# Performance work log

Measured on AMD Instinct MI355X. Metric: run time of the kernel, lower is better.

The kernel has to match this reference:

```python
import jax, jax.numpy as jnp
import numpy as np

PRESERVE_RATIO = 0.8
TEMPERATURE = 1.5


def setup_inputs() -> dict:
    key = jax.random.key(0)
    ks = jax.random.split(key, 8)
    B, C, H, W = 2, 64, 96, 96
    inter = C // 2
    bott = C // 4
    s = 0.02
    return {
        "x": jax.random.normal(ks[0], (B, C, H, W), dtype=jnp.float32),
        "g_w": jax.random.normal(ks[1], (inter, C), dtype=jnp.float32) * s,
        "theta_w": jax.random.normal(ks[2], (inter, C), dtype=jnp.float32) * s,
        "phi_w": jax.random.normal(ks[3], (inter, C), dtype=jnp.float32) * s,
        "W_w": jax.random.normal(ks[4], (C, inter), dtype=jnp.float32) * s,
        "cg1_w": jax.random.normal(ks[5], (bott, C), dtype=jnp.float32) * s,
        "cg1_b": jnp.zeros((bott,), dtype=jnp.float32),
        "cg2_w": jax.random.normal(ks[6], (C, bott), dtype=jnp.float32) * s,
        "cg2_b": jnp.zeros((C,), dtype=jnp.float32),
    }


def reference(x, g_w, theta_w, phi_w, W_w, cg1_w, cg1_b, cg2_w, cg2_b):
    B, C, H, W = x.shape
    N = H * W
    # color gate: global avg pool -> 1x1 conv -> relu -> 1x1 conv -> sigmoid
    pooled = jnp.mean(x, axis=(2, 3))                       # [B, C]
    h = jax.nn.relu(pooled @ cg1_w.T + cg1_b)               # [B, C//4]
    gate = jax.nn.sigmoid(h @ cg2_w.T + cg2_b)              # [B, C]

    xf = x.reshape(B, C, N)                                 # [B, C, N]
    g_x = jnp.einsum('ic,bcn->bni', g_w, xf)                # [B, N, I]
    theta = jnp.einsum('ic,bcn->bni', theta_w, xf)          # [B, N, I]
    phi = jnp.einsum('ic,bcn->bin', phi_w, xf)              # [B, I, N]

    affinity = jnp.einsum('bni,bim->bnm', theta, phi) / TEMPERATURE  # [B, N, N]
    affinity = jax.nn.softmax(affinity, axis=-1)
    y = jnp.einsum('bnm,bmi->bni', affinity, g_x)           # [B, N, I]
    y = jnp.einsum('ci,bni->bcn', W_w, y).reshape(B, C, H, W)
    y = y * gate[:, :, None, None] * PRESERVE_RATIO
    return x + y
```

## Files before the change

### kernel.cpp

```cpp
#include <hip/hip_runtime.h>

#define N_TOK 9216
#define C_DIM 64
#define I_DIM 32
#define BOT 16
#define B_SZ 2
#define N_TILES 144

typedef short bf16x8 __attribute__((ext_vector_type(8)));
typedef float f32x4 __attribute__((ext_vector_type(4)));
typedef float f32x16 __attribute__((ext_vector_type(16)));

#define KST 36
#define VST 68

__device__ __forceinline__ unsigned packbf(float a, float b) {
  return __builtin_amdgcn_perm(__float_as_uint(b), __float_as_uint(a), 0x07060302u);
}
__device__ __forceinline__ unsigned short bftrunc(float f) {
  return (unsigned short)(__float_as_uint(f) >> 16);
}
__device__ __forceinline__ float bflo(unsigned u) {
  return __uint_as_float(u << 16);
}
__device__ __forceinline__ float bfhi(unsigned u) {
  return __uint_as_float(u & 0xffff0000u);
}

__global__ __launch_bounds__(256) void proj_pool_kernel(
    const float* __restrict__ x, const float* __restrict__ g_w,
    const float* __restrict__ theta_w, const float* __restrict__ phi_w,
    unsigned short* __restrict__ Q, unsigned short* __restrict__ K,
    unsigned short* __restrict__ VT, float* __restrict__ pooled) {
  if (blockIdx.x >= 216) {
    int bc = blockIdx.x - 216;
    const float* p = x + (size_t)bc * N_TOK;
    float s = 0.f;
    for (int t = threadIdx.x; t < N_TOK; t += 256) s += p[t];
#pragma unroll
    for (int off = 32; off >= 1; off >>= 1) s += __shfl_down(s, off, 64);
    __shared__ float red[4];
    int wid = threadIdx.x >> 6, lane = threadIdx.x & 63;
    if (lane == 0) red[wid] = s;
    __syncthreads();
    if (threadIdx.x == 0)
      pooled[bc] = (red[0] + red[1] + red[2] + red[3]) * (1.0f / N_TOK);
    return;
  }
  const int lane = threadIdx.x & 63;
  const int m = lane & 15, quad = lane >> 4;
  int task = blockIdx.x * 4 + (threadIdx.x >> 6);
  int mat = task / 288;
  int r0 = task % 288;
  int b = r0 / 144;
  int n0 = (r0 % 144) * 64;
  const float* wsrc = (mat == 0) ? theta_w : ((mat == 1) ? phi_w : g_w);
  const float scale = (mat == 0) ? 0.96179669439f : 1.0f;

  bf16x8 afr[2][2];
#pragma unroll
  for (int it = 0; it < 2; ++it)
#pragma unroll
    for (int cs = 0; cs < 2; ++cs) {
      const float* wp = wsrc + (it * 16 + m) * C_DIM + cs * 32 + quad * 8;
      union { unsigned u[4]; bf16x8 v; } t;
#pragma unroll
      for (int j = 0; j < 4; ++j)
        t.u[j] = packbf(wp[2 * j] * scale, wp[2 * j + 1] * scale);
      afr[it][cs] = t.v;
    }

#pragma unroll
  for (int sub = 0; sub < 4; ++sub) {
    const int ns = n0 + sub * 16;
    const float* xb = x + (size_t)b * C_DIM * N_TOK + ns + m;
    bf16x8 bfr[2];
#pragma unroll
    for (int cs = 0; cs < 2; ++cs) {
      union { unsigned u[4]; bf16x8 v; } t;
#pragma unroll
      for (int j = 0; j < 4; ++j) {
        float v0 = xb[(size_t)(cs * 32 + quad * 8 + 2 * j) * N_TOK];
        float v1 = xb[(size_t)(cs * 32 + quad * 8 + 2 * j + 1) * N_TOK];
        t.u[j] = packbf(v0, v1);
      }
      bfr[cs] = t.v;
    }

    f32x4 acc[2] = {{0.f, 0.f, 0.f, 0.f}, {0.f, 0.f, 0.f, 0.f}};
#pragma unroll
    for (int cs = 0; cs < 2; ++cs)
#pragma unroll
      for (int it = 0; it < 2; ++it)
        acc[it] = __builtin_amdgcn_mfma_f32_16x16x32_bf16(afr[it][cs], bfr[cs],
                                                          acc[it], 0, 0, 0);
    if (mat < 2) {
      unsigned short* dst =
          ((mat == 0) ? Q : K) + ((size_t)b * N_TOK + ns + m) * I_DIM;
#pragma unroll
      for (int it = 0; it < 2; ++it) {
        unsigned u0 = packbf(acc[it][0], acc[it][1]);
        unsigned u1 = packbf(acc[it][2], acc[it][3]);
        *(uint2*)(dst + it * 16 + quad * 4) = make_uint2(u0, u1);
      }
    } else {
#pragma unroll
      for (int it = 0; it < 2; ++it)
#pragma unroll
        for (int r = 0; r < 4; ++r)
          VT[((size_t)b * I_DIM + it * 16 + quad * 4 + r) * N_TOK + ns + m] =
              bftrunc(acc[it][r]);
    }
  }
}

__device__ __forceinline__ void tilework(const f32x16 s, const bf16x8 bvA,
                                         const bf16x8 bvB, f32x16& accy,
                                         float& lsum) {
  float e[16];
#pragma unroll
  for (int r = 0; r < 16; ++r) e[r] = __builtin_amdgcn_exp2f(s[r]);
  float l0 = 0.f, l1 = 0.f, l2 = 0.f, l3 = 0.f;
#pragma unroll
  for (int r = 0; r < 4; ++r) {
    l0 += e[r]; l1 += e[4 + r]; l2 += e[8 + r]; l3 += e[12 + r];
  }
  lsum += (l0 + l1) + (l2 + l3);
  unsigned pk[8];
#pragma unroll
  for (int i = 0; i < 8; ++i) pk[i] = packbf(e[2 * i], e[2 * i + 1]);
  asm("v_permlane32_swap_b32 %0, %1" : "+v"(pk[0]), "+v"(pk[2]));
  asm("v_permlane32_swap_b32 %0, %1" : "+v"(pk[1]), "+v"(pk[3]));
  asm("v_permlane32_swap_b32 %0, %1" : "+v"(pk[4]), "+v"(pk[6]));
  asm("v_permlane32_swap_b32 %0, %1" : "+v"(pk[5]), "+v"(pk[7]));
  union { unsigned u[4]; bf16x8 v; } A0, A1;
  A0.u[0] = pk[0]; A0.u[1] = pk[1]; A0.u[2] = pk[2]; A0.u[3] = pk[3];
  A1.u[0] = pk[4]; A1.u[1] = pk[5]; A1.u[2] = pk[6]; A1.u[3] = pk[7];
  accy = __builtin_amdgcn_mfma_f32_32x32x16_bf16(A0.v, bvA, accy, 0, 0, 0);
  accy = __builtin_amdgcn_mfma_f32_32x32x16_bf16(A1.v, bvB, accy, 0, 0, 0);
}

__device__ __forceinline__ bf16x8 lds_frag(const unsigned short* p) {
  union { uint2 d[2]; bf16x8 v; } t;
  t.d[0] = *(const uint2*)(p);
  t.d[1] = *(const uint2*)(p + 4);
  return t.v;
}

__global__ __launch_bounds__(256, 4) void attn_kernel(
    const unsigned short* __restrict__ Q, const unsigned short* __restrict__ Kg,
    const unsigned short* __restrict__ VT, unsigned short* __restrict__ Ypart,
    float* __restrict__ Lpart, int tps) {
  const int tid = threadIdx.x;
  const int lane = tid & 63;
  const int l32 = lane & 31, h = lane >> 5;
  const int ks = blockIdx.y, b = blockIdx.z;
  const int q0 = blockIdx.x * 128 + (tid >> 6) * 32;
  const unsigned short* Qb = Q + (size_t)b * N_TOK * I_DIM;
  const unsigned short* Kb = Kg + (size_t)b * N_TOK * I_DIM;
  const unsigned short* Vb = VT + (size_t)b * I_DIM * N_TOK;

  __shared__ __align__(16) unsigned short Ks[64 * KST];
  __shared__ __align__(16) unsigned short Vs[32 * VST];

  bf16x8 bq0 = *(const bf16x8*)(Qb + (size_t)(q0 + l32) * I_DIM + h * 8);
  bf16x8 bq1 = *(const bf16x8*)(Qb + (size_t)(q0 + l32) * I_DIM + 16 + h * 8);

  f32x16 accy = {};
  float lsum = 0.f;
  const f32x16 zz = {};

  const int kt0 = ks * tps;
  const int kr = tid >> 2, kc = (tid & 3) * 8;
  const int vr = tid >> 3, vc = (tid & 7) * 8;
  const unsigned short* kgp = Kb + ((size_t)kt0 * 64 + kr) * I_DIM + kc;
  const unsigned short* vgp = Vb + (size_t)vr * N_TOK + kt0 * 64 + vc;
  unsigned short* klp = &Ks[kr * KST + kc];
  unsigned short* vlp = &Vs[vr * VST + vc];

  {
    uint4 rk = *(const uint4*)kgp;
    uint4 rv = *(const uint4*)vgp;
    *(uint2*)(klp) = make_uint2(rk.x, rk.y);
    *(uint2*)(klp + 4) = make_uint2(rk.z, rk.w);
    *(uint2*)(vlp) = make_uint2(rv.x, rv.y);
    *(uint2*)(vlp + 4) = make_uint2(rv.z, rv.w);
  }

  for (int kt = 0; kt < tps; ++kt) {
    __syncthreads();
    const bool pf = (kt + 1 < tps);
    uint4 rk = {0, 0, 0, 0}, rv = {0, 0, 0, 0};
    if (pf) {
      rk = *(const uint4*)(kgp + (size_t)(kt + 1) * 64 * I_DIM);
      rv = *(const uint4*)(vgp + (kt + 1) * 64);
    }
    asm volatile("" ::: "memory");

    bf16x8 ak00 = lds_frag(&Ks[l32 * KST + 8 * h]);
    bf16x8 ak01 = lds_frag(&Ks[l32 * KST + 16 + 8 * h]);
    bf16x8 ak10 = lds_frag(&Ks[(32 + l32) * KST + 8 * h]);
    bf16x8 ak11 = lds_frag(&Ks[(32 + l32) * KST + 16 + 8 * h]);
    bf16x8 bv0 = lds_frag(&Vs[l32 * VST + 8 * h]);
    bf16x8 bv1 = lds_frag(&Vs[l32 * VST + 16 + 8 * h]);
    bf16x8 bv2 = lds_frag(&Vs[l32 * VST + 32 + 8 * h]);
    bf16x8 bv3 = lds_frag(&Vs[l32 * VST + 48 + 8 * h]);

    f32x16 s0 = __builtin_amdgcn_mfma_f32_32x32x16_bf16(ak00, bq0, zz, 0, 0, 0);
    s0 = __builtin_amdgcn_mfma_f32_32x32x16_bf16(ak01, bq1, s0, 0, 0, 0);
    f32x16 s1 = __builtin_amdgcn_mfma_f32_32x32x16_bf16(ak10, bq0, zz, 0, 0, 0);
    s1 = __builtin_amdgcn_mfma_f32_32x32x16_bf16(ak11, bq1, s1, 0, 0, 0);

    tilework(s0, bv0, bv1, accy, lsum);
    tilework(s1, bv2, bv3, accy, lsum);

    __syncthreads();
    if (pf) {
      *(uint2*)(klp) = make_uint2(rk.x, rk.y);
      *(uint2*)(klp + 4) = make_uint2(rk.z, rk.w);
      *(uint2*)(vlp) = make_uint2(rv.x, rv.y);
      *(uint2*)(vlp + 4) = make_uint2(rv.z, rv.w);
    }
  }

  lsum += __shfl_xor(lsum, 32, 64);

  const size_t base = (size_t)(ks * B_SZ + b) * N_TOK + q0;
#pragma unroll
  for (int R = 0; R < 4; ++R)
#pragma unroll
    for (int r = 0; r < 4; ++r)
      Ypart[(base + r + 8 * R + 4 * h) * I_DIM + l32] = bftrunc(accy[4 * R + r]);
  if (h == 0) Lpart[base + l32] = lsum;
}

__global__ __launch_bounds__(256) void epilogue_kernel(
    const float* __restrict__ x, const float* __restrict__ W_w,
    const float* __restrict__ pooled, const float* __restrict__ cg1_w,
    const float* __restrict__ cg1_b, const float* __restrict__ cg2_w,
    const float* __restrict__ cg2_b, const unsigned short* __restrict__ Ypart,
    const float* __restrict__ Lpart, float* __restrict__ out, int KS) {
  __shared__ float Ysh[64][33];
  __shared__ float lsh[64];
  __shared__ float gsh[64];
  __shared__ float hl[BOT];
  const int t = threadIdx.x;
  const int b = blockIdx.y;
  const int n0 = blockIdx.x * 64;

  if (t < BOT) {
    float a = cg1_b[t];
#pragma unroll
    for (int c = 0; c < C_DIM; ++c)
      a += cg1_w[t * C_DIM + c] * pooled[b * C_DIM + c];
    hl[t] = a > 0.f ? a : 0.f;
  }

  {
    int nl = t >> 2, i0 = (t & 3) * 8;
    float s[8];
#pragma unroll
    for (int k = 0; k < 8; ++k) s[k] = 0.f;
    for (int ks = 0; ks < KS; ++ks) {
      const unsigned short* yp =
          Ypart + ((size_t)(ks * B_SZ + b) * N_TOK + n0 + nl) * I_DIM + i0;
      uint4 v = *(const uint4*)yp;
      s[0] += bflo(v.x); s[1] += bfhi(v.x);
      s[2] += bflo(v.y); s[3] += bfhi(v.y);
      s[4] += bflo(v.z); s[5] += bfhi(v.z);
      s[6] += bflo(v.w); s[7] += bfhi(v.w);
    }
#pragma unroll
    for (int k = 0; k < 8; ++k) Ysh[nl][i0 + k] = s[k];
    if (t < 64) {
      float ls = 0.f;
      for (int ks = 0; ks < KS; ++ks)
        ls += Lpart[(size_t)(ks * B_SZ + b) * N_TOK + n0 + t];
      lsh[t] = ls;
    }
  }
  __syncthreads();

  if (t < C_DIM) {
    float z = cg2_b[t];
#pragma unroll
    for (int j = 0; j < BOT; ++j) z += cg2_w[t * BOT + j] * hl[j];
    gsh[t] = 0.8f / (1.f + __expf(-z));
  }
  __syncthreads();

  const int n = t & 63, cg = t >> 6;
  float y[I_DIM];
#pragma unroll
  for (int i = 0; i < I_DIM; ++i) y[i] = Ysh[n][i];
  const float inv = 1.0f / lsh[n];
  const float* xb = x + ((size_t)b * C_DIM + cg * 16) * N_TOK + n0 + n;
  float* ob = out + ((size_t)b * C_DIM + cg * 16) * N_TOK + n0 + n;
#pragma unroll
  for (int c16 = 0; c16 < 16; ++c16) {
    const int c = cg * 16 + c16;
    float sacc = 0.f;
#pragma unroll
    for (int i = 0; i < I_DIM; ++i) sacc += W_w[c * I_DIM + i] * y[i];
    ob[(size_t)c16 * N_TOK] = xb[(size_t)c16 * N_TOK] + gsh[c] * inv * sacc;
  }
}

extern "C" void kernel_launch(void* const* d_in, const int* in_sizes, int n_in,
                              void* d_out, int out_size, void* d_ws, size_t ws_size,
                              hipStream_t stream) {
  const float* x = (const float*)d_in[0];
  const float* g_w = (const float*)d_in[1];
  const float* theta_w = (const float*)d_in[2];
  const float* phi_w = (const float*)d_in[3];
  const float* W_w = (const float*)d_in[4];
  const float* cg1_w = (const float*)d_in[5];
  const float* cg1_b = (const float*)d_in[6];
  const float* cg2_w = (const float*)d_in[7];
  const float* cg2_b = (const float*)d_in[8];
  float* out = (float*)d_out;

  char* w = (char*)d_ws;
  const size_t bfsz = (size_t)B_SZ * N_TOK * I_DIM * sizeof(unsigned short);
  unsigned short* Qb = (unsigned short*)(w);
  unsigned short* Kb = (unsigned short*)(w + bfsz);
  unsigned short* VT = (unsigned short*)(w + 2 * bfsz);
  float* pooled = (float*)(w + 3 * bfsz);
  char* w2 = w + 3 * bfsz + 8192;

  int KS = 16;
  {
    const size_t per = (size_t)B_SZ * N_TOK * (I_DIM * 2 + 4);
    while (KS > 1 && (3 * bfsz + 8192 + (size_t)KS * per) > ws_size) KS >>= 1;
  }
  float* Lpart = (float*)w2;
  unsigned short* Ypart =
      (unsigned short*)(w2 + (size_t)KS * B_SZ * N_TOK * sizeof(float));
  int tps = N_TILES / KS;

  proj_pool_kernel<<<dim3(344), 256, 0, stream>>>(x, g_w, theta_w, phi_w, Qb,
                                                  Kb, VT, pooled);
  attn_kernel<<<dim3(72, KS, B_SZ), 256, 0, stream>>>(Qb, Kb, VT, Ypart, Lpart, tps);
  epilogue_kernel<<<dim3(N_TOK / 64, B_SZ), 256, 0, stream>>>(
      x, W_w, pooled, cg1_w, cg1_b, cg2_w, cg2_b, Ypart, Lpart, out, KS);
}
```

Baseline: 142.2 us.

## Double-buffer K/V LDS tiles with two-deep prefetch and 128-bit LDS access

Measured after the change: 147.0 us. +3.3%, slower.

```diff
diff --git a/kernel.cpp b/kernel.cpp
--- a/kernel.cpp
+++ b/kernel.cpp
@@ -11,8 +11,8 @@
 typedef float f32x4 __attribute__((ext_vector_type(4)));
 typedef float f32x16 __attribute__((ext_vector_type(16)));
 
-#define KST 36
-#define VST 68
+#define KST 40
+#define VST 72
 
 __device__ __forceinline__ unsigned packbf(float a, float b) {
   return __builtin_amdgcn_perm(__float_as_uint(b), __float_as_uint(a), 0x07060302u);
@@ -20,12 +20,8 @@
 __device__ __forceinline__ unsigned short bftrunc(float f) {
   return (unsigned short)(__float_as_uint(f) >> 16);
 }
-__device__ __forceinline__ float bflo(unsigned u) {
-  return __uint_as_float(u << 16);
-}
-__device__ __forceinline__ float bfhi(unsigned u) {
-  return __uint_as_float(u & 0xffff0000u);
-}
+__device__ __forceinline__ float bflo(unsigned u) { return __uint_as_float(u << 16); }
+__device__ __forceinline__ float bfhi(unsigned u) { return __uint_as_float(u & 0xffff0000u); }
 
 __global__ __launch_bounds__(256) void proj_pool_kernel(
     const float* __restrict__ x, const float* __restrict__ g_w,
@@ -138,13 +134,6 @@
   A1.u[0] = pk[4]; A1.u[1] = pk[5]; A1.u[2] = pk[6]; A1.u[3] = pk[7];
   accy = __builtin_amdgcn_mfma_f32_32x32x16_bf16(A0.v, bvA, accy, 0, 0, 0);
   accy = __builtin_amdgcn_mfma_f32_32x32x16_bf16(A1.v, bvB, accy, 0, 0, 0);
-}
-
-__device__ __forceinline__ bf16x8 lds_frag(const unsigned short* p) {
-  union { uint2 d[2]; bf16x8 v; } t;
-  t.d[0] = *(const uint2*)(p);
-  t.d[1] = *(const uint2*)(p + 4);
-  return t.v;
 }
 
 __global__ __launch_bounds__(256, 4) void attn_kernel(
@@ -160,8 +149,8 @@
   const unsigned short* Kb = Kg + (size_t)b * N_TOK * I_DIM;
   const unsigned short* Vb = VT + (size_t)b * I_DIM * N_TOK;
 
-  __shared__ __align__(16) unsigned short Ks[64 * KST];
-  __shared__ __align__(16) unsigned short Vs[32 * VST];
+  __shared__ __align__(16) unsigned short Ks[2][64 * KST];
+  __shared__ __align__(16) unsigned short Vs[2][32 * VST];
 
   bf16x8 bq0 = *(const bf16x8*)(Qb + (size_t)(q0 + l32) * I_DIM + h * 8);
   bf16x8 bq1 = *(const bf16x8*)(Qb + (size_t)(q0 + l32) * I_DIM + 16 + h * 8);
@@ -175,36 +164,37 @@
   const int vr = tid >> 3, vc = (tid & 7) * 8;
   const unsigned short* kgp = Kb + ((size_t)kt0 * 64 + kr) * I_DIM + kc;
   const unsigned short* vgp = Vb + (size_t)vr * N_TOK + kt0 * 64 + vc;
-  unsigned short* klp = &Ks[kr * KST + kc];
-  unsigned short* vlp = &Vs[vr * VST + vc];
 
   {
-    uint4 rk = *(const uint4*)kgp;
-    uint4 rv = *(const uint4*)vgp;
-    *(uint2*)(klp) = make_uint2(rk.x, rk.y);
-    *(uint2*)(klp + 4) = make_uint2(rk.z, rk.w);
-    *(uint2*)(vlp) = make_uint2(rv.x, rv.y);
-    *(uint2*)(vlp + 4) = make_uint2(rv.z, rv.w);
-  }
+    uint4 r0k = *(const uint4*)kgp;
+    uint4 r0v = *(const uint4*)vgp;
+    *(uint4*)&Ks[0][kr * KST + kc] = r0k;
+    *(uint4*)&Vs[0][vr * VST + vc] = r0v;
+  }
+  uint4 rk = {0, 0, 0, 0}, rv = {0, 0, 0, 0};
+  if (tps > 1) {
+    rk = *(const uint4*)(kgp + 64 * I_DIM);
+    rv = *(const uint4*)(vgp + 64);
+  }
+  __syncthreads();
 
   for (int kt = 0; kt < tps; ++kt) {
-    __syncthreads();
-    const bool pf = (kt + 1 < tps);
-    uint4 rk = {0, 0, 0, 0}, rv = {0, 0, 0, 0};
-    if (pf) {
-      rk = *(const uint4*)(kgp + (size_t)(kt + 1) * 64 * I_DIM);
-      rv = *(const uint4*)(vgp + (kt + 1) * 64);
+    const int p = kt & 1;
+    uint4 rk2 = {0, 0, 0, 0}, rv2 = {0, 0, 0, 0};
+    if (kt + 2 < tps) {
+      rk2 = *(const uint4*)(kgp + (size_t)(kt + 2) * 64 * I_DIM);
+      rv2 = *(const uint4*)(vgp + (kt + 2) * 64);
     }
     asm volatile("" ::: "memory");
 
-    bf16x8 ak00 = lds_frag(&Ks[l32 * KST + 8 * h]);
-    bf16x8 ak01 = lds_frag(&Ks[l32 * KST + 16 + 8 * h]);
-    bf16x8 ak10 = lds_frag(&Ks[(32 + l32) * KST + 8 * h]);
-    bf16x8 ak11 = lds_frag(&Ks[(32 + l32) * KST + 16 + 8 * h]);
-    bf16x8 bv0 = lds_frag(&Vs[l32 * VST + 8 * h]);
-    bf16x8 bv1 = lds_frag(&Vs[l32 * VST + 16 + 8 * h]);
-    bf16x8 bv2 = lds_frag(&Vs[l32 * VST + 32 + 8 * h]);
-    bf16x8 bv3 = lds_frag(&Vs[l32 * VST + 48 + 8 * h]);
+    bf16x8 ak00 = *(const bf16x8*)&Ks[p][l32 * KST + 8 * h];
+    bf16x8 ak01 = *(const bf16x8*)&Ks[p][l32 * KST + 16 + 8 * h];
+    bf16x8 ak10 = *(const bf16x8*)&Ks[p][(32 + l32) * KST + 8 * h];
+    bf16x8 ak11 = *(const bf16x8*)&Ks[p][(32 + l32) * KST + 16 + 8 * h];
+    bf16x8 bv0 = *(const bf16x8*)&Vs[p][l32 * VST + 8 * h];
+    bf16x8 bv1 = *(const bf16x8*)&Vs[p][l32 * VST + 16 + 8 * h];
+    bf16x8 bv2 = *(const bf16x8*)&Vs[p][l32 * VST + 32 + 8 * h];
+    bf16x8 bv3 = *(const bf16x8*)&Vs[p][l32 * VST + 48 + 8 * h];
 
     f32x16 s0 = __builtin_amdgcn_mfma_f32_32x32x16_bf16(ak00, bq0, zz, 0, 0, 0);
     s0 = __builtin_amdgcn_mfma_f32_32x32x16_bf16(ak01, bq1, s0, 0, 0, 0);
@@ -214,13 +204,12 @@
     tilework(s0, bv0, bv1, accy, lsum);
     tilework(s1, bv2, bv3, accy, lsum);
 
+    if (kt + 1 < tps) {
+      *(uint4*)&Ks[1 - p][kr * KST + kc] = rk;
+      *(uint4*)&Vs[1 - p][vr * VST + vc] = rv;
+    }
+    rk = rk2; rv = rv2;
     __syncthreads();
-    if (pf) {
-      *(uint2*)(klp) = make_uint2(rk.x, rk.y);
-      *(uint2*)(klp + 4) = make_uint2(rk.z, rk.w);
-      *(uint2*)(vlp) = make_uint2(rv.x, rv.y);
-      *(uint2*)(vlp + 4) = make_uint2(rv.z, rv.w);
-    }
   }
 
   lsum += __shfl_xor(lsum, 32, 64);
```
